# Performance work log

Hardware: AMD Instinct MI355X
Metric: run time of the kernel (lower is better)

## Reference

```python
import jax, jax.numpy as jnp
import numpy as np

B, D, H, L = 2048, 4096, 1024, 64
LAM = 1.0  # topo_lambda


def setup_inputs() -> dict:
    key = jax.random.key(0)
    ks = jax.random.split(key, 5)
    def w(k, sh):
        fan_in = sh[0]
        return (jax.random.normal(k, sh, jnp.float32) * (1.0 / fan_in) ** 0.5)
    return {
        "x": jax.random.normal(ks[0], (B, D), jnp.float32),
        "W1": w(ks[1], (D, H)), "b1": jnp.zeros((H,), jnp.float32),
        "W2": w(ks[2], (H, L)), "b2": jnp.zeros((L,), jnp.float32),
        "W3": w(ks[3], (L, H)), "b3": jnp.zeros((H,), jnp.float32),
        "W4": w(ks[4], (H, D)), "b4": jnp.zeros((D,), jnp.float32),
        "latent_norm": jnp.ones((1,), jnp.float32),
    }


def _cdist(a):
    # pairwise euclidean distances [N, N], safe sqrt (zero grad on zero diag)
    sq = jnp.sum(a * a, axis=1)
    d2 = jnp.maximum(sq[:, None] + sq[None, :] - 2.0 * (a @ a.T), 0.0)
    pos = d2 > 0
    return jnp.where(pos, jnp.sqrt(jnp.where(pos, d2, 1.0)), 0.0)


def _mst_edges(d):
    # 0-dim persistence pairs == MST edges of the dense distance matrix.
    # Vectorized Prim's algorithm: scan of N-1 steps, O(N) work per step.
    n = d.shape[0]
    in_tree = jnp.zeros((n,), bool).at[0].set(True)
    min_dist = d[0]
    parent = jnp.zeros((n,), jnp.int32)

    def step(carry, _):
        in_tree, min_dist, parent = carry
        j = jnp.argmin(jnp.where(in_tree, jnp.inf, min_dist)).astype(jnp.int32)
        i = parent[j]
        in_tree = in_tree.at[j].set(True)
        better = (d[j] < min_dist) & ~in_tree
        min_dist = jnp.where(better, d[j], min_dist)
        parent = jnp.where(better, j, parent)
        return (in_tree, min_dist, parent), jnp.stack([i, j])

    _, edges = jax.lax.scan(step, (in_tree, min_dist, parent), None, length=n - 1)
    return edges  # [n-1, 2] int32


def _topo_signature(dx, dz):
    # pairing indices computed on detached distances (as in torch .detach())
    p1 = _mst_edges(jax.lax.stop_gradient(dx))
    p2 = _mst_edges(jax.lax.stop_gradient(dz))
    sig1 = dx[p1[:, 0], p1[:, 1]]
    sig1_2 = dz[p1[:, 0], p1[:, 1]]
    sig2 = dz[p2[:, 0], p2[:, 1]]
    sig2_1 = dx[p2[:, 0], p2[:, 1]]
    # match_edges == 'symmetric'
    return jnp.sum((sig1 - sig1_2) ** 2) + jnp.sum((sig2 - sig2_1) ** 2)


def reference(x, W1, b1, W2, b2, W3, b3, W4, b4, latent_norm):
    z = jax.nn.relu(x @ W1 + b1) @ W2 + b2            # [B, L]
    x_rec = jax.nn.relu(z @ W3 + b3) @ W4 + b4        # [B, D]
    rec_loss = jnp.mean((x_rec - x) ** 2)
    x_dist = _cdist(x)
    x_dist = x_dist / jnp.max(x_dist)
    z_dist = _cdist(z) / latent_norm[0]
    topo_loss = _topo_signature(x_dist, z_dist) / x.shape[0]
    loss = rec_loss + LAM * topo_loss
    return loss
```

## Files before the change

kernel.cpp:

```cpp
#include <hip/hip_runtime.h>
#include <hip/hip_bf16.h>

#define B_N 2048
#define D_N 4096
#define H_N 1024
#define L_N 64
#define NTILE 136
#define SPLK 8

typedef __attribute__((ext_vector_type(8))) short short8;
typedef __attribute__((ext_vector_type(4))) float float4_t;

#define ASG __attribute__((address_space(1)))
#define ASL __attribute__((address_space(3)))

__device__ inline float bf2f(unsigned short u) {
  union { unsigned u; float f; } v; v.u = ((unsigned)u) << 16; return v.f;
}
__device__ inline unsigned short f2bf(float f) {
  union { float f; unsigned u; } v; v.f = f;
  unsigned r = v.u + 0x7fffu + ((v.u >> 16) & 1u);
  return (unsigned short)(r >> 16);
}

__device__ inline float block_sum256(float v) {
  const int lane = threadIdx.x & 63, wave = threadIdx.x >> 6;
#pragma unroll
  for (int off = 32; off; off >>= 1) v += __shfl_xor(v, off);
  __shared__ float red_s[4];
  if (lane == 0) red_s[wave] = v;
  __syncthreads();
  return red_s[0] + red_s[1] + red_s[2] + red_s[3];
}

__device__ inline float block_max256(float v) {
  const int lane = threadIdx.x & 63, wave = threadIdx.x >> 6;
#pragma unroll
  for (int off = 32; off; off >>= 1) v = fmaxf(v, __shfl_xor(v, off));
  __shared__ float redm_s[4];
  if (lane == 0) redm_s[wave] = v;
  __syncthreads();
  return fmaxf(fmaxf(redm_s[0], redm_s[1]), fmaxf(redm_s[2], redm_s[3]));
}

__device__ inline void tri_idx(int b, int& tm, int& tn) {
  int m = (int)((sqrtf(8.f * (float)b + 1.f) - 1.f) * 0.5f);
  while ((m + 1) * (m + 2) / 2 <= b) ++m;
  while (m * (m + 1) / 2 > b) --m;
  tm = m;
  tn = b - m * (m + 1) / 2;
}


__global__ __launch_bounds__(256) void prep_x(const float* __restrict__ x,
                                              unsigned short* __restrict__ xb,
                                              float* __restrict__ sqx) {
  const int row = blockIdx.x;
  const int t = threadIdx.x;
  const float4* xr = (const float4*)(x + (size_t)row * D_N);
  ushort4* xbr = (ushort4*)(xb + (size_t)row * D_N);
  float s = 0.f;
  for (int i = t; i < D_N / 4; i += 256) {
    float4 v = xr[i];
    s += v.x * v.x + v.y * v.y + v.z * v.z + v.w * v.w;
    ushort4 o;
    o.x = f2bf(v.x); o.y = f2bf(v.y); o.z = f2bf(v.z); o.w = f2bf(v.w);
    xbr[i] = o;
  }
  float tot = block_sum256(s);
  if (t == 0) sqx[row] = tot;
}

__global__ __launch_bounds__(256) void transpose_cast(const float* __restrict__ in,
                                                      unsigned short* __restrict__ out,
                                                      int R, int C) {
  __shared__ float tile[32][33];
  const int c0 = blockIdx.x * 32, r0 = blockIdx.y * 32;
  const int tx = threadIdx.x, ty = threadIdx.y;
#pragma unroll
  for (int i = 0; i < 32; i += 8)
    tile[ty + i][tx] = in[(size_t)(r0 + ty + i) * C + c0 + tx];
  __syncthreads();
#pragma unroll
  for (int i = 0; i < 32; i += 8)
    out[(size_t)(c0 + ty + i) * R + r0 + tx] = f2bf(tile[tx][ty + i]);
}

__global__ __launch_bounds__(1024) void init_bor(float* __restrict__ accum,
                                                 int* __restrict__ comp,
                                                 int* __restrict__ cnt,
                                                 int* __restrict__ done) {
  const int t = threadIdx.x;
  if (t < 2) { accum[t] = 0.f; cnt[t] = 0; done[t] = 0; }
  for (int v = t; v < 2 * B_N; v += 1024) comp[v] = v & (B_N - 1);
}


__device__ inline void gemm_mainloop(const unsigned short* __restrict__ A,
                                     const unsigned short* __restrict__ Bt,
                                     int ld, int Klen, int m_base, int n_base,
                                     float4_t acc[4][4]) {
  __shared__ unsigned short lA[128 * 32];
  __shared__ unsigned short lB[128 * 32];
  const int t = threadIdx.x;
  const int wave = t >> 6;
  const int lane = t & 63;
  const int lrow = lane & 15;
  const int quad = lane >> 4;
  const int wm = (wave & 1) * 64;
  const int wn = (wave >> 1) * 64;

  const int srow = lane >> 2;
  const int scol = (lane & 3) * 8;

  for (int k0 = 0; k0 < Klen; k0 += 32) {
    __syncthreads();
#pragma unroll
    for (int q = 0; q < 2; ++q) {
      const int rbase = wave * 32 + q * 16;
      const int row = rbase + srow;
      __builtin_amdgcn_global_load_lds(
          (ASG void*)(A + (size_t)(m_base + row) * ld + k0 + scol),
          (ASL void*)(lA + rbase * 32), 16, 0, 0);
      __builtin_amdgcn_global_load_lds(
          (ASG void*)(Bt + (size_t)(n_base + row) * ld + k0 + scol),
          (ASL void*)(lB + rbase * 32), 16, 0, 0);
    }
    __syncthreads();
    short8 af[4], bfr[4];
#pragma unroll
    for (int f = 0; f < 4; ++f) {
      af[f]  = *(const short8*)(lA + (wm + f * 16 + lrow) * 32 + quad * 8);
      bfr[f] = *(const short8*)(lB + (wn + f * 16 + lrow) * 32 + quad * 8);
    }
#pragma unroll
    for (int fm = 0; fm < 4; ++fm)
#pragma unroll
      for (int fn = 0; fn < 4; ++fn)
        acc[fm][fn] = __builtin_amdgcn_mfma_f32_16x16x32_bf16(af[fm], bfr[fn],
                                                              acc[fm][fn], 0, 0, 0);
  }
}

__global__ __launch_bounds__(256) void gemm_splitk(const unsigned short* __restrict__ A,
                                                   const unsigned short* __restrict__ Bt,
                                                   int ld, int Kchunk, int N,
                                                   float* __restrict__ partial) {
  float4_t acc[4][4];
  float4_t z4 = {0.f, 0.f, 0.f, 0.f};
#pragma unroll
  for (int a = 0; a < 4; ++a)
#pragma unroll
    for (int b = 0; b < 4; ++b) acc[a][b] = z4;
  const int s = blockIdx.z;
  const int m_base = blockIdx.y * 128, n_base = blockIdx.x * 128;
  gemm_mainloop(A + (size_t)s * Kchunk, Bt + (size_t)s * Kchunk, ld, Kchunk,
                m_base, n_base, acc);
  const size_t MN = (size_t)gridDim.y * 128 * N;
  float* __restrict__ P = partial + (size_t)s * MN;
  const int t = threadIdx.x, wave = t >> 6, lane = t & 63;
  const int lrow = lane & 15, quad = lane >> 4;
  const int wm = (wave & 1) * 64, wn = (wave >> 1) * 64;
#pragma unroll
  for (int fm = 0; fm < 4; ++fm)
#pragma unroll
    for (int fn = 0; fn < 4; ++fn) {
      const int r0 = m_base + wm + fm * 16 + quad * 4;
      const int c = n_base + wn + fn * 16 + lrow;
#pragma unroll
      for (int r = 0; r < 4; ++r)
        P[(size_t)(r0 + r) * N + c] = acc[fm][fn][r];
    }
}

__global__ __launch_bounds__(256) void gemm_d2_tri(const unsigned short* __restrict__ xb,
                                                   float* __restrict__ partial) {
  float4_t acc[4][4];
  float4_t z4 = {0.f, 0.f, 0.f, 0.f};
#pragma unroll
  for (int a = 0; a < 4; ++a)
#pragma unroll
    for (int b = 0; b < 4; ++b) acc[a][b] = z4;
  const int s = blockIdx.z;
  int tm, tn;
  tri_idx(blockIdx.x, tm, tn);
  gemm_mainloop(xb + (size_t)s * (D_N / SPLK), xb + (size_t)s * (D_N / SPLK), D_N,
                D_N / SPLK, tm * 128, tn * 128, acc);
  float* __restrict__ P = partial + ((size_t)s * NTILE + blockIdx.x) * 16384;
  const int t = threadIdx.x, wave = t >> 6, lane = t & 63;
  const int lrow = lane & 15, quad = lane >> 4;
  const int wm = (wave & 1) * 64, wn = (wave >> 1) * 64;
#pragma unroll
  for (int fm = 0; fm < 4; ++fm)
#pragma unroll
    for (int fn = 0; fn < 4; ++fn) {
      const int lr0 = wm + fm * 16 + quad * 4;
      const int lc = wn + fn * 16 + lrow;
#pragma unroll
      for (int r = 0; r < 4; ++r)
        P[(lr0 + r) * 128 + lc] = acc[fm][fn][r];
    }
}

__global__ __launch_bounds__(256) void fin_bias_relu(const float* __restrict__ partial,
                                                     const float* __restrict__ bias,
                                                     unsigned short* __restrict__ out) {
  const size_t MN = (size_t)B_N * H_N;
  const size_t i4 = ((size_t)blockIdx.x * 256 + threadIdx.x) * 4;
  float4 a = *(const float4*)(partial + i4);
#pragma unroll
  for (int s = 1; s < SPLK; ++s) {
    float4 p = *(const float4*)(partial + s * MN + i4);
    a.x += p.x; a.y += p.y; a.z += p.z; a.w += p.w;
  }
  const int c = (int)(i4 & (H_N - 1));
  float4 b = *(const float4*)(bias + c);
  ushort4 o;
  o.x = f2bf(fmaxf(a.x + b.x, 0.f));
  o.y = f2bf(fmaxf(a.y + b.y, 0.f));
  o.z = f2bf(fmaxf(a.z + b.z, 0.f));
  o.w = f2bf(fmaxf(a.w + b.w, 0.f));
  *(ushort4*)(out + i4) = o;
}

__global__ __launch_bounds__(256) void fin_d2_tri(const float* __restrict__ partial,
                                                  const float* __restrict__ sq,
                                                  float* __restrict__ Out,
                                                  unsigned* __restrict__ max_slot) {
  const int tile = blockIdx.y;
  const int c0 = blockIdx.x * 32;
  int tm, tn;
  tri_idx(tile, tm, tn);
  __shared__ float lds[32][132];
  const int t = threadIdx.x;
  const int cc = (t & 7) * 4;
  float lmax = 0.f;
#pragma unroll
  for (int q = 0; q < 4; ++q) {
    const int r = (t >> 3) + 32 * q;
    const float* base = partial + (size_t)tile * 16384 + r * 128 + c0 + cc;
    float4 a = *(const float4*)base;
#pragma unroll
    for (int s = 1; s < SPLK; ++s) {
      float4 p = *(const float4*)(base + (size_t)s * NTILE * 16384);
      a.x += p.x; a.y += p.y; a.z += p.z; a.w += p.w;
    }
    const int i = tm * 128 + r;
    const float si = sq[i];
    float4 sj = *(const float4*)(sq + tn * 128 + c0 + cc);
    float4 v;
    v.x = fmaxf(si + sj.x - 2.f * a.x, 0.f);
    v.y = fmaxf(si + sj.y - 2.f * a.y, 0.f);
    v.z = fmaxf(si + sj.z - 2.f * a.z, 0.f);
    v.w = fmaxf(si + sj.w - 2.f * a.w, 0.f);
    *(float4*)(Out + (size_t)i * B_N + tn * 128 + c0 + cc) = v;
    lds[cc + 0][r] = v.x;
    lds[cc + 1][r] = v.y;
    lds[cc + 2][r] = v.z;
    lds[cc + 3][r] = v.w;
    lmax = fmaxf(lmax, fmaxf(fmaxf(v.x, v.y), fmaxf(v.z, v.w)));
  }
  __syncthreads();
#pragma unroll
  for (int m = 0; m < 4; ++m) {
    const int lin = t + 256 * m;
    const int cc2 = lin >> 5;
    const int r4 = (lin & 31) * 4;
    float4 w = *(const float4*)(&lds[cc2][r4]);
    *(float4*)(Out + (size_t)(tn * 128 + c0 + cc2) * B_N + tm * 128 + r4) = w;
  }
  float tot = block_max256(lmax);
  if (t == 0) atomicMax(max_slot, __float_as_uint(tot));
}

__global__ __launch_bounds__(256) void gemm_recloss(const unsigned short* __restrict__ A,
                                                    const unsigned short* __restrict__ Bt,
                                                    const float* __restrict__ bias,
                                                    const float* __restrict__ Xref,
                                                    float* __restrict__ acc_slot,
                                                    int K, int N) {
  float4_t acc[4][4];
  float4_t z4 = {0.f, 0.f, 0.f, 0.f};
#pragma unroll
  for (int a = 0; a < 4; ++a)
#pragma unroll
    for (int b = 0; b < 4; ++b) acc[a][b] = z4;
  const int m_base = blockIdx.y * 128, n_base = blockIdx.x * 128;
  gemm_mainloop(A, Bt, K, K, m_base, n_base, acc);
  const int t = threadIdx.x, wave = t >> 6, lane = t & 63;
  const int lrow = lane & 15, quad = lane >> 4;
  const int wm = (wave & 1) * 64, wn = (wave >> 1) * 64;
  float local = 0.f;
#pragma unroll
  for (int fm = 0; fm < 4; ++fm)
#pragma unroll
    for (int fn = 0; fn < 4; ++fn) {
      const int r0 = m_base + wm + fm * 16 + quad * 4;
      const int c = n_base + wn + fn * 16 + lrow;
      const float bc = bias[c];
#pragma unroll
      for (int r = 0; r < 4; ++r) {
        float v = acc[fm][fn][r] + bc - Xref[(size_t)(r0 + r) * N + c];
        local += v * v;
      }
    }
  float tot = block_sum256(local);
  if (t == 0) atomicAdd(acc_slot, tot);
}


__global__ __launch_bounds__(256) void g2_k(const unsigned short* __restrict__ h1b,
                                            const float* __restrict__ W2,
                                            const float* __restrict__ b2,
                                            float* __restrict__ z,
                                            float* __restrict__ sqz) {
  const int col = threadIdx.x & 63;
  const int row = blockIdx.x * 4 + (threadIdx.x >> 6);
  const unsigned short* hr = h1b + (size_t)row * H_N;
  float a0 = 0.f, a1 = 0.f, a2 = 0.f, a3 = 0.f;
  for (int k = 0; k < H_N; k += 4) {
    a0 += bf2f(hr[k + 0]) * W2[(k + 0) * L_N + col];
    a1 += bf2f(hr[k + 1]) * W2[(k + 1) * L_N + col];
    a2 += bf2f(hr[k + 2]) * W2[(k + 2) * L_N + col];
    a3 += bf2f(hr[k + 3]) * W2[(k + 3) * L_N + col];
  }
  const float zv = (a0 + a1) + (a2 + a3) + b2[col];
  z[(size_t)row * L_N + col] = zv;
  float s = zv * zv;
#pragma unroll
  for (int off = 32; off; off >>= 1) s += __shfl_xor(s, off);
  if (col == 0) sqz[row] = s;
}

__global__ __launch_bounds__(256) void g3_k(const float* __restrict__ z,
                                            const float* __restrict__ W3,
                                            const float* __restrict__ b3,
                                            unsigned short* __restrict__ h2b) {
  const int t = threadIdx.x;
  const int col = blockIdx.y * 256 + t;
  const int r0 = blockIdx.x * 4;
  __shared__ float zr[4][64];
  zr[t >> 6][t & 63] = z[(size_t)(r0 + (t >> 6)) * L_N + (t & 63)];
  __syncthreads();
  const float bc = b3[col];
  float a0 = bc, a1 = bc, a2 = bc, a3 = bc;
#pragma unroll 8
  for (int k = 0; k < 64; ++k) {
    float w = W3[k * H_N + col];
    a0 += zr[0][k] * w;
    a1 += zr[1][k] * w;
    a2 += zr[2][k] * w;
    a3 += zr[3][k] * w;
  }
  h2b[(size_t)(r0 + 0) * H_N + col] = f2bf(fmaxf(a0, 0.f));
  h2b[(size_t)(r0 + 1) * H_N + col] = f2bf(fmaxf(a1, 0.f));
  h2b[(size_t)(r0 + 2) * H_N + col] = f2bf(fmaxf(a2, 0.f));
  h2b[(size_t)(r0 + 3) * H_N + col] = f2bf(fmaxf(a3, 0.f));
}

__global__ __launch_bounds__(256) void d2z_k(const float* __restrict__ z,
                                             const float* __restrict__ sqz,
                                             float* __restrict__ d2z) {
  const int bi = blockIdx.y * 16, bj = blockIdx.x * 16;
  __shared__ float zi[16][65], zj[16][65];
  const int t = threadIdx.x;
  for (int idx = t; idx < 16 * 64; idx += 256) {
    const int r = idx >> 6, c = idx & 63;
    zi[r][c] = z[(size_t)(bi + r) * L_N + c];
    zj[r][c] = z[(size_t)(bj + r) * L_N + c];
  }
  __syncthreads();
  const int ti = t >> 4, tj = t & 15;
  float dot = 0.f;
#pragma unroll 8
  for (int k = 0; k < 64; ++k) dot += zi[ti][k] * zj[tj][k];
  float v = fmaxf(sqz[bi + ti] + sqz[bj + tj] - 2.f * dot, 0.f);
  d2z[(size_t)(bi + ti) * B_N + bj + tj] = v;
}

__global__ __launch_bounds__(256) void bor_scan(const float* __restrict__ d2x,
                                                const float* __restrict__ d2z,
                                                const int* __restrict__ comp,
                                                unsigned long long* __restrict__ rowbest,
                                                const int* __restrict__ done) {
  const int tree = blockIdx.y;
  if (done[tree]) return;
  const float* __restrict__ d2 = tree ? d2z : d2x;
  const int* __restrict__ cp = comp + tree * B_N;
  const int i = blockIdx.x;
  const int t = threadIdx.x;
  const int ci = cp[i];
  const float* __restrict__ row = d2 + (size_t)i * B_N;
  const unsigned ibase = (unsigned)(i << 11);
  unsigned long long k = ~0ull;
#pragma unroll
  for (int m = 0; m < 2; ++m) {
    const int j4 = (t + m * 256) * 4;
    float4 dv = *(const float4*)(row + j4);
    int4 cj = *(const int4*)(cp + j4);
    if (cj.x != ci) {
      unsigned long long key = (((unsigned long long)__float_as_uint(dv.x)) << 32) | (ibase | (unsigned)(j4 + 0));
      k = key < k ? key : k;
    }
    if (cj.y != ci) {
      unsigned long long key = (((unsigned long long)__float_as_uint(dv.y)) << 32) | (ibase | (unsigned)(j4 + 1));
      k = key < k ? key : k;
    }
    if (cj.z != ci) {
      unsigned long long key = (((unsigned long long)__float_as_uint(dv.z)) << 32) | (ibase | (unsigned)(j4 + 2));
      k = key < k ? key : k;
    }
    if (cj.w != ci) {
      unsigned long long key = (((unsigned long long)__float_as_uint(dv.w)) << 32) | (ibase | (unsigned)(j4 + 3));
      k = key < k ? key : k;
    }
  }
  const int lane = t & 63, wave = t >> 6;
#pragma unroll
  for (int off = 32; off; off >>= 1) {
    unsigned long long o = __shfl_xor(k, off);
    k = o < k ? o : k;
  }
  __shared__ unsigned long long wmin[4];
  if (lane == 0) wmin[wave] = k;
  __syncthreads();
  if (t == 0) {
    unsigned long long a = wmin[0] < wmin[1] ? wmin[0] : wmin[1];
    unsigned long long b = wmin[2] < wmin[3] ? wmin[2] : wmin[3];
    rowbest[tree * B_N + i] = (a < b) ? a : b;
  }
}

__global__ __launch_bounds__(1024) void bor_merge(const unsigned long long* __restrict__ rowbest,
                                                  int* __restrict__ comp,
                                                  int2* __restrict__ edges,
                                                  int* __restrict__ cnt,
                                                  int* __restrict__ done) {
  const int tree = blockIdx.x;
  if (done[tree]) return;
  const unsigned long long* __restrict__ rb = rowbest + tree * B_N;
  int* __restrict__ cp = comp + tree * B_N;
  int2* __restrict__ eo = edges + (size_t)tree * (B_N - 1);
  int* __restrict__ cn = cnt + tree;
  __shared__ unsigned long long bc[B_N];
  __shared__ int hk[B_N];
  __shared__ int allsame;
  const int t = threadIdx.x;

#pragma unroll
  for (int q = 0; q < 2; ++q) bc[t + q * 1024] = ~0ull;
  __syncthreads();

#pragma unroll
  for (int q = 0; q < 2; ++q) {
    const int i = t + q * 1024;
    const unsigned long long key = rb[i];
    if (key != ~0ull) atomicMin(&bc[cp[i]], key);
  }
  __syncthreads();

  unsigned long long mykey[2];
#pragma unroll
  for (int q = 0; q < 2; ++q) {
    const int c = t + q * 1024;
    const unsigned long long key = bc[c];
    mykey[q] = key;
    int h = c;
    if (key != ~0ull) h = cp[(unsigned)key & (unsigned)(B_N - 1)];
    hk[c] = h;
  }
  __syncthreads();

  int rloc[2];
#pragma unroll
  for (int q = 0; q < 2; ++q) {
    const int c = t + q * 1024;
    const unsigned long long key = mykey[q];
    const int h = hk[c];
    const int hh = hk[h];
    const bool valid = key != ~0ull;
    const bool two = (h != c) && (hh == c);
    rloc[q] = (two && c < h) ? c : h;
    if (valid && (!two || c < h)) {
      int e = atomicAdd(cn, 1);
      eo[e] = make_int2((int)((key >> 11) & (unsigned)(B_N - 1)),
                        (int)(key & (unsigned)(B_N - 1)));
    }
  }
  __syncthreads();
#pragma unroll
  for (int q = 0; q < 2; ++q) hk[t + q * 1024] = rloc[q];
  if (t == 0) allsame = 1;
  __syncthreads();

  for (int it = 0; it < 11; ++it) {
    const int v0 = hk[hk[t]];
    const int v1 = hk[hk[t + 1024]];
    __syncthreads();
    hk[t] = v0;
    hk[t + 1024] = v1;
    __syncthreads();
  }

#pragma unroll
  for (int q = 0; q < 2; ++q) {
    const int v = t + q * 1024;
    cp[v] = hk[cp[v]];
  }
  __syncthreads();
  const int c0v = cp[0];
  if (cp[t] != c0v || cp[t + 1024] != c0v) allsame = 0;
  __syncthreads();
  if (t == 0 && allsame) done[tree] = 1;
}

__global__ __launch_bounds__(256) void final_k(const float* __restrict__ d2x,
                                               const float* __restrict__ d2z,
                                               const int2* __restrict__ edges,
                                               const float* __restrict__ accum,
                                               const float* __restrict__ latent_norm,
                                               float* __restrict__ out) {
  const int t = threadIdx.x;
  const float maxd = sqrtf(__uint_as_float(((const unsigned*)accum)[1]));
  const float inv_maxd = 1.0f / maxd;
  const float inv_ln = 1.0f / latent_norm[0];
  float local = 0.f;
  for (int e = t; e < 2 * (B_N - 1); e += 256) {
    int2 ij = edges[e];
    size_t idx = (size_t)ij.x * B_N + ij.y;
    float xd = sqrtf(d2x[idx]) * inv_maxd;
    float zd = sqrtf(d2z[idx]) * inv_ln;
    float d = xd - zd;
    local += d * d;
  }
  float topo = block_sum256(local);
  if (t == 0)
    out[0] = accum[0] * (1.0f / ((float)B_N * (float)D_N)) + topo * (1.0f / (float)B_N);
}

extern "C" void kernel_launch(void* const* d_in, const int* in_sizes, int n_in,
                              void* d_out, int out_size, void* d_ws, size_t ws_size,
                              hipStream_t stream) {
  const float* x  = (const float*)d_in[0];
  const float* W1 = (const float*)d_in[1];
  const float* b1 = (const float*)d_in[2];
  const float* W2 = (const float*)d_in[3];
  const float* b2 = (const float*)d_in[4];
  const float* W3 = (const float*)d_in[5];
  const float* b3 = (const float*)d_in[6];
  const float* W4 = (const float*)d_in[7];
  const float* b4 = (const float*)d_in[8];
  const float* latent_norm = (const float*)d_in[9];
  float* out = (float*)d_out;

  char* ws = (char*)d_ws;
  size_t off = 0;
  auto alloc = [&](size_t bytes) {
    size_t o = off;
    off += (bytes + 255) & ~(size_t)255;
    return o;
  };
  unsigned short* xb   = (unsigned short*)(ws + alloc((size_t)B_N * D_N * 2));
  unsigned short* w1bt = (unsigned short*)(ws + alloc((size_t)H_N * D_N * 2));
  unsigned short* w4bt = (unsigned short*)(ws + alloc((size_t)D_N * H_N * 2));
  unsigned short* h1b  = (unsigned short*)(ws + alloc((size_t)B_N * H_N * 2));
  unsigned short* h2b  = (unsigned short*)(ws + alloc((size_t)B_N * H_N * 2));
  float* z    = (float*)(ws + alloc((size_t)B_N * L_N * 4));
  float* sqx  = (float*)(ws + alloc((size_t)B_N * 4));
  float* sqz  = (float*)(ws + alloc((size_t)B_N * 4));
  float* d2x  = (float*)(ws + alloc((size_t)B_N * B_N * 4));
  float* d2z  = (float*)(ws + alloc((size_t)B_N * B_N * 4));
  int2* edges = (int2*)(ws + alloc((size_t)2 * (B_N - 1) * sizeof(int2)));
  float* accum = (float*)(ws + alloc(256));
  int* comp   = (int*)(ws + alloc((size_t)2 * B_N * 4));
  unsigned long long* rowbest = (unsigned long long*)(ws + alloc((size_t)2 * B_N * 8));
  int* cnt    = (int*)(ws + alloc(256));
  int* done   = (int*)(ws + alloc(256));
  float* parts = (float*)(ws + alloc((size_t)SPLK * NTILE * 16384 * 4));

  init_bor<<<1, 1024, 0, stream>>>(accum, comp, cnt, done);
  prep_x<<<B_N, 256, 0, stream>>>(x, xb, sqx);
  transpose_cast<<<dim3(H_N / 32, D_N / 32), dim3(32, 8), 0, stream>>>(W1, w1bt, D_N, H_N);
  transpose_cast<<<dim3(D_N / 32, H_N / 32), dim3(32, 8), 0, stream>>>(W4, w4bt, H_N, D_N);

  gemm_splitk<<<dim3(H_N / 128, B_N / 128, SPLK), 256, 0, stream>>>(xb, w1bt, D_N,
                                                                    D_N / SPLK, H_N, parts);
  fin_bias_relu<<<(B_N * H_N) / 1024, 256, 0, stream>>>(parts, b1, h1b);

  g2_k<<<B_N / 4, 256, 0, stream>>>(h1b, W2, b2, z, sqz);
  g3_k<<<dim3(B_N / 4, H_N / 256), 256, 0, stream>>>(z, W3, b3, h2b);
  gemm_recloss<<<dim3(D_N / 128, B_N / 128), 256, 0, stream>>>(h2b, w4bt, b4, x, accum, H_N, D_N);

  gemm_d2_tri<<<dim3(NTILE, 1, SPLK), 256, 0, stream>>>(xb, parts);
  fin_d2_tri<<<dim3(4, NTILE), 256, 0, stream>>>(parts, sqx, d2x, (unsigned*)(accum + 1));

  d2z_k<<<dim3(B_N / 16, B_N / 16), 256, 0, stream>>>(z, sqz, d2z);

  for (int r = 0; r < 11; ++r) {
    bor_scan<<<dim3(B_N, 2), 256, 0, stream>>>(d2x, d2z, comp, rowbest, done);
    bor_merge<<<2, 1024, 0, stream>>>(rowbest, comp, edges, cnt, done);
  }
  final_k<<<1, 256, 0, stream>>>(d2x, d2z, edges, accum, latent_norm, out);
}
```

Before: 434.8 us.

## Store bf16 GEMM operands in K-panel-major layout and halve split-K

All bf16 GEMM operands (xb, transposed W1/W4, h1b, h2b) are rewritten into a panel layout of 32-wide K slices, [K/32][rows][32]. Each 128x32 tile load then reads one contiguous 8 KB block instead of 128 rows strided by the full K. Producers (prep_x, transpose_cast, fin_bias_relu, g3_k) and consumers (the GEMM mainloop, g2_k) are updated to match. Split-K drops from 8 to 4, which cuts partial-sum traffic and reduction work but gives fewer blocks for parallelism.

```diff
diff --git a/kernel.cpp b/kernel.cpp
--- a/kernel.cpp
+++ b/kernel.cpp
@@ -6,13 +6,14 @@
 #define H_N 1024
 #define L_N 64
 #define NTILE 136
-#define SPLK 8
+#define SPLK 4
 
 typedef __attribute__((ext_vector_type(8))) short short8;
 typedef __attribute__((ext_vector_type(4))) float float4_t;
 
 #define ASG __attribute__((address_space(1)))
 #define ASL __attribute__((address_space(3)))
+
 
 __device__ inline float bf2f(unsigned short u) {
   union { unsigned u; float f; } v; v.u = ((unsigned)u) << 16; return v.f;
@@ -58,14 +59,15 @@
   const int row = blockIdx.x;
   const int t = threadIdx.x;
   const float4* xr = (const float4*)(x + (size_t)row * D_N);
-  ushort4* xbr = (ushort4*)(xb + (size_t)row * D_N);
   float s = 0.f;
   for (int i = t; i < D_N / 4; i += 256) {
     float4 v = xr[i];
     s += v.x * v.x + v.y * v.y + v.z * v.z + v.w * v.w;
     ushort4 o;
     o.x = f2bf(v.x); o.y = f2bf(v.y); o.z = f2bf(v.z); o.w = f2bf(v.w);
-    xbr[i] = o;
+    const int p = i >> 3;
+    const int k31 = (4 * i) & 31;
+    *(ushort4*)(xb + ((size_t)p * B_N + row) * 32 + k31) = o;
   }
   float tot = block_sum256(s);
   if (t == 0) sqx[row] = tot;
@@ -83,7 +85,7 @@
   __syncthreads();
 #pragma unroll
   for (int i = 0; i < 32; i += 8)
-    out[(size_t)(c0 + ty + i) * R + r0 + tx] = f2bf(tile[tx][ty + i]);
+    out[((size_t)(r0 >> 5) * C + c0 + ty + i) * 32 + tx] = f2bf(tile[tx][ty + i]);
 }
 
 __global__ __launch_bounds__(1024) void init_bor(float* __restrict__ accum,
@@ -98,7 +100,7 @@
 
 __device__ inline void gemm_mainloop(const unsigned short* __restrict__ A,
                                      const unsigned short* __restrict__ Bt,
-                                     int ld, int Klen, int m_base, int n_base,
+                                     int nrA, int nrB, int Klen, int m_base, int n_base,
                                      float4_t acc[4][4]) {
   __shared__ unsigned short lA[128 * 32];
   __shared__ unsigned short lB[128 * 32];
@@ -114,16 +116,18 @@
   const int scol = (lane & 3) * 8;
 
   for (int k0 = 0; k0 < Klen; k0 += 32) {
+    const size_t pA = (size_t)(k0 >> 5) * nrA;
+    const size_t pB = (size_t)(k0 >> 5) * nrB;
     __syncthreads();
 #pragma unroll
     for (int q = 0; q < 2; ++q) {
       const int rbase = wave * 32 + q * 16;
       const int row = rbase + srow;
       __builtin_amdgcn_global_load_lds(
-          (ASG void*)(A + (size_t)(m_base + row) * ld + k0 + scol),
+          (ASG void*)(A + (pA + m_base + row) * 32 + scol),
           (ASL void*)(lA + rbase * 32), 16, 0, 0);
       __builtin_amdgcn_global_load_lds(
-          (ASG void*)(Bt + (size_t)(n_base + row) * ld + k0 + scol),
+          (ASG void*)(Bt + (pB + n_base + row) * 32 + scol),
           (ASL void*)(lB + rbase * 32), 16, 0, 0);
     }
     __syncthreads();
@@ -144,7 +148,7 @@
 
 __global__ __launch_bounds__(256) void gemm_splitk(const unsigned short* __restrict__ A,
                                                    const unsigned short* __restrict__ Bt,
-                                                   int ld, int Kchunk, int N,
+                                                   int nrA, int nrB, int Kchunk, int N,
                                                    float* __restrict__ partial) {
   float4_t acc[4][4];
   float4_t z4 = {0.f, 0.f, 0.f, 0.f};
@@ -154,7 +158,8 @@
     for (int b = 0; b < 4; ++b) acc[a][b] = z4;
   const int s = blockIdx.z;
   const int m_base = blockIdx.y * 128, n_base = blockIdx.x * 128;
-  gemm_mainloop(A + (size_t)s * Kchunk, Bt + (size_t)s * Kchunk, ld, Kchunk,
+  const size_t po = (size_t)(s * (Kchunk >> 5));
+  gemm_mainloop(A + po * nrA * 32, Bt + po * nrB * 32, nrA, nrB, Kchunk,
                 m_base, n_base, acc);
   const size_t MN = (size_t)gridDim.y * 128 * N;
   float* __restrict__ P = partial + (size_t)s * MN;
@@ -184,8 +189,8 @@
   const int s = blockIdx.z;
   int tm, tn;
   tri_idx(blockIdx.x, tm, tn);
-  gemm_mainloop(xb + (size_t)s * (D_N / SPLK), xb + (size_t)s * (D_N / SPLK), D_N,
-                D_N / SPLK, tm * 128, tn * 128, acc);
+  const size_t po = (size_t)(s * ((D_N / SPLK) >> 5)) * B_N * 32;
+  gemm_mainloop(xb + po, xb + po, B_N, B_N, D_N / SPLK, tm * 128, tn * 128, acc);
   float* __restrict__ P = partial + ((size_t)s * NTILE + blockIdx.x) * 16384;
   const int t = threadIdx.x, wave = t >> 6, lane = t & 63;
   const int lrow = lane & 15, quad = lane >> 4;
@@ -213,14 +218,15 @@
     float4 p = *(const float4*)(partial + s * MN + i4);
     a.x += p.x; a.y += p.y; a.z += p.z; a.w += p.w;
   }
-  const int c = (int)(i4 & (H_N - 1));
-  float4 b = *(const float4*)(bias + c);
+  const int row = (int)(i4 >> 10);
+  const int k = (int)(i4 & (H_N - 1));
+  float4 b = *(const float4*)(bias + k);
   ushort4 o;
   o.x = f2bf(fmaxf(a.x + b.x, 0.f));
   o.y = f2bf(fmaxf(a.y + b.y, 0.f));
   o.z = f2bf(fmaxf(a.z + b.z, 0.f));
   o.w = f2bf(fmaxf(a.w + b.w, 0.f));
-  *(ushort4*)(out + i4) = o;
+  *(ushort4*)(out + ((size_t)(k >> 5) * B_N + row) * 32 + (k & 31)) = o;
 }
 
 __global__ __launch_bounds__(256) void fin_d2_tri(const float* __restrict__ partial,
@@ -277,8 +283,7 @@
                                                     const unsigned short* __restrict__ Bt,
                                                     const float* __restrict__ bias,
                                                     const float* __restrict__ Xref,
-                                                    float* __restrict__ acc_slot,
-                                                    int K, int N) {
+                                                    float* __restrict__ acc_slot) {
   float4_t acc[4][4];
   float4_t z4 = {0.f, 0.f, 0.f, 0.f};
 #pragma unroll
@@ -286,7 +291,7 @@
 #pragma unroll
     for (int b = 0; b < 4; ++b) acc[a][b] = z4;
   const int m_base = blockIdx.y * 128, n_base = blockIdx.x * 128;
-  gemm_mainloop(A, Bt, K, K, m_base, n_base, acc);
+  gemm_mainloop(A, Bt, B_N, D_N, H_N, m_base, n_base, acc);
   const int t = threadIdx.x, wave = t >> 6, lane = t & 63;
   const int lrow = lane & 15, quad = lane >> 4;
   const int wm = (wave & 1) * 64, wn = (wave >> 1) * 64;
@@ -300,7 +305,7 @@
       const float bc = bias[c];
 #pragma unroll
       for (int r = 0; r < 4; ++r) {
-        float v = acc[fm][fn][r] + bc - Xref[(size_t)(r0 + r) * N + c];
+        float v = acc[fm][fn][r] + bc - Xref[(size_t)(r0 + r) * D_N + c];
         local += v * v;
       }
     }
@@ -316,13 +321,17 @@
                                             float* __restrict__ sqz) {
   const int col = threadIdx.x & 63;
   const int row = blockIdx.x * 4 + (threadIdx.x >> 6);
-  const unsigned short* hr = h1b + (size_t)row * H_N;
   float a0 = 0.f, a1 = 0.f, a2 = 0.f, a3 = 0.f;
-  for (int k = 0; k < H_N; k += 4) {
-    a0 += bf2f(hr[k + 0]) * W2[(k + 0) * L_N + col];
-    a1 += bf2f(hr[k + 1]) * W2[(k + 1) * L_N + col];
-    a2 += bf2f(hr[k + 2]) * W2[(k + 2) * L_N + col];
-    a3 += bf2f(hr[k + 3]) * W2[(k + 3) * L_N + col];
+  for (int p = 0; p < H_N / 32; ++p) {
+    const unsigned short* hb = h1b + ((size_t)p * B_N + row) * 32;
+    const float* wb = W2 + (p * 32) * L_N + col;
+#pragma unroll
+    for (int k2 = 0; k2 < 32; k2 += 4) {
+      a0 += bf2f(hb[k2 + 0]) * wb[(k2 + 0) * L_N];
+      a1 += bf2f(hb[k2 + 1]) * wb[(k2 + 1) * L_N];
+      a2 += bf2f(hb[k2 + 2]) * wb[(k2 + 2) * L_N];
+      a3 += bf2f(hb[k2 + 3]) * wb[(k2 + 3) * L_N];
+    }
   }
   const float zv = (a0 + a1) + (a2 + a3) + b2[col];
   z[(size_t)row * L_N + col] = zv;
@@ -352,10 +361,11 @@
     a2 += zr[2][k] * w;
     a3 += zr[3][k] * w;
   }
-  h2b[(size_t)(r0 + 0) * H_N + col] = f2bf(fmaxf(a0, 0.f));
-  h2b[(size_t)(r0 + 1) * H_N + col] = f2bf(fmaxf(a1, 0.f));
-  h2b[(size_t)(r0 + 2) * H_N + col] = f2bf(fmaxf(a2, 0.f));
-  h2b[(size_t)(r0 + 3) * H_N + col] = f2bf(fmaxf(a3, 0.f));
+  const size_t base = ((size_t)(col >> 5) * B_N) * 32 + (col & 31);
+  h2b[base + (size_t)(r0 + 0) * 32] = f2bf(fmaxf(a0, 0.f));
+  h2b[base + (size_t)(r0 + 1) * 32] = f2bf(fmaxf(a1, 0.f));
+  h2b[base + (size_t)(r0 + 2) * 32] = f2bf(fmaxf(a2, 0.f));
+  h2b[base + (size_t)(r0 + 3) * 32] = f2bf(fmaxf(a3, 0.f));
 }
 
 __global__ __launch_bounds__(256) void d2z_k(const float* __restrict__ z,
@@ -583,13 +593,13 @@
   transpose_cast<<<dim3(H_N / 32, D_N / 32), dim3(32, 8), 0, stream>>>(W1, w1bt, D_N, H_N);
   transpose_cast<<<dim3(D_N / 32, H_N / 32), dim3(32, 8), 0, stream>>>(W4, w4bt, H_N, D_N);
 
-  gemm_splitk<<<dim3(H_N / 128, B_N / 128, SPLK), 256, 0, stream>>>(xb, w1bt, D_N,
-                                                                    D_N / SPLK, H_N, parts);
+  gemm_splitk<<<dim3(H_N / 128, B_N / 128, SPLK), 256, 0, stream>>>(
+      xb, w1bt, B_N, H_N, D_N / SPLK, H_N, parts);
   fin_bias_relu<<<(B_N * H_N) / 1024, 256, 0, stream>>>(parts, b1, h1b);
 
   g2_k<<<B_N / 4, 256, 0, stream>>>(h1b, W2, b2, z, sqz);
   g3_k<<<dim3(B_N / 4, H_N / 256), 256, 0, stream>>>(z, W3, b3, h2b);
-  gemm_recloss<<<dim3(D_N / 128, B_N / 128), 256, 0, stream>>>(h2b, w4bt, b4, x, accum, H_N, D_N);
+  gemm_recloss<<<dim3(D_N / 128, B_N / 128), 256, 0, stream>>>(h2b, w4bt, b4, x, accum);
 
   gemm_d2_tri<<<dim3(NTILE, 1, SPLK), 256, 0, stream>>>(xb, parts);
   fin_d2_tri<<<dim3(4, NTILE), 256, 0, stream>>>(parts, sqx, d2x, (unsigned*)(accum + 1));
```

Measured after the change: 427.2 us. About the same (-1.7%).
